# Optimization experiments

Measured on AMD Instinct MI355X. Metric: run time of the kernel, lower is better.

## Reference

```python
import jax, jax.numpy as jnp
import numpy as np

N, F, H, C, CLS = 100000, 128, 4, 32, 2
E = 1600000
NEG_SLOPE = 0.2


def setup_inputs() -> dict:
    key = jax.random.key(0)
    ks = jax.random.split(key, 8)
    x = jax.random.normal(ks[0], (N, F), dtype=jnp.float32)
    edge_index = jax.random.randint(ks[1], (2, E), 0, N, dtype=jnp.int64)
    # GATConv params (PyG layout): lin weight [H*C, F], att vectors [H, C], bias [H*C]
    W_gat = jax.random.normal(ks[2], (H * C, F), dtype=jnp.float32) * (1.0 / np.sqrt(F))
    att_src = jax.random.normal(ks[3], (H, C), dtype=jnp.float32) * (1.0 / np.sqrt(C))
    att_dst = jax.random.normal(ks[4], (H, C), dtype=jnp.float32) * (1.0 / np.sqrt(C))
    b_gat = jnp.zeros((H * C,), dtype=jnp.float32)
    # final classifier Linear(H*C -> CLS)
    W_lin = jax.random.normal(ks[5], (CLS, H * C), dtype=jnp.float32) * (1.0 / np.sqrt(H * C))
    b_lin = jnp.zeros((CLS,), dtype=jnp.float32)
    return {"x": x, "edge_index": edge_index, "W_gat": W_gat, "att_src": att_src,
            "att_dst": att_dst, "b_gat": b_gat, "W_lin": W_lin, "b_lin": b_lin}


def _gat_conv(x, edge_index, W_gat, att_src, att_dst, b_gat):
    # add self loops (PyG default add_self_loops=True)
    loop = jnp.arange(N, dtype=edge_index.dtype)
    src = jnp.concatenate([edge_index[0], loop])  # [E+N]
    dst = jnp.concatenate([edge_index[1], loop])
    h = (x @ W_gat.T).reshape(N, H, C)            # [N, H, C]
    a_src = jnp.einsum('nhc,hc->nh', h, att_src)  # [N, H]
    a_dst = jnp.einsum('nhc,hc->nh', h, att_dst)
    e = a_src[src] + a_dst[dst]                   # [E+N, H]
    e = jnp.where(e >= 0, e, NEG_SLOPE * e)       # leaky_relu(0.2)
    # segment softmax over incoming edges of each destination node
    m = jax.ops.segment_max(e, dst, num_segments=N)          # [N, H]
    ex = jnp.exp(e - m[dst])                                  # [E+N, H]
    denom = jax.ops.segment_sum(ex, dst, num_segments=N)      # [N, H]
    alpha = ex / denom[dst]                                    # [E+N, H]
    msg = alpha[:, :, None] * h[src]                           # [E+N, H, C]
    out = jax.ops.segment_sum(msg, dst, num_segments=N)       # [N, H, C]
    return out.reshape(N, H * C) + b_gat


def reference(x, edge_index, W_gat, att_src, att_dst, b_gat, W_lin, b_lin):
    out = _gat_conv(x, edge_index, W_gat, att_src, att_dst, b_gat)
    out = jax.nn.relu(out)
    return out @ W_lin.T + b_lin  # [N, CLS]
```

## Files before the change

kernel.cpp:

```cpp
#include <hip/hip_runtime.h>

#define NSLOPE  0.2f
#define LEXP(v) __expf((v) >= 0.f ? (v) : NSLOPE * (v))

typedef __attribute__((ext_vector_type(8))) short bf16x8;
typedef __attribute__((ext_vector_type(4))) float f32x4;

__device__ __forceinline__ unsigned bf16_rne(float f) {
    unsigned x = __float_as_uint(f);
    return (x + 0x7fffu + ((x >> 16) & 1u)) >> 16;
}
__device__ __forceinline__ float bf_lo(unsigned u) { return __uint_as_float(u << 16); }
__device__ __forceinline__ float bf_hi(unsigned u) { return __uint_as_float(u & 0xffff0000u); }

__global__ __launch_bounds__(256) void k_gemm_init(
    const float* __restrict__ x, const float* __restrict__ Wg,
    const float* __restrict__ att_src, const float* __restrict__ att_dst,
    unsigned* __restrict__ h2, float* __restrict__ a_src, float* __restrict__ a_dst,
    int N, int* __restrict__ gcur, int nbkt, int cap)
{
    __shared__ unsigned short Wl[128 * 136];
    __shared__ unsigned short wattH[8][128];

    const int t = threadIdx.x;

    if (blockIdx.x >= 512) {
        for (int i = t; i < nbkt; i += 256) gcur[i] = i * cap;
        return;
    }

    for (int i = t; i < 128 * 32; i += 256) {
        int r = i >> 5, c4 = (i & 31) * 4;
        float4 w = *(const float4*)(Wg + r * 128 + c4);
        unsigned* wp = (unsigned*)((char*)Wl + r * 272 + c4 * 2);
        wp[0] = bf16_rne(w.x) | (bf16_rne(w.y) << 16);
        wp[1] = bf16_rne(w.z) | (bf16_rne(w.w) << 16);
    }
    for (int idx = t; idx < 1024; idx += 256) {
        int j = idx >> 7, f = idx & 127;
        const float* av = (j < 4) ? (att_src + j * 32) : (att_dst + (j - 4) * 32);
        int hh = (j & 3) * 32;
        float s = 0.f;
        #pragma unroll 8
        for (int k = 0; k < 32; ++k)
            s += av[k] * Wg[(size_t)(hh + k) * 128 + f];
        wattH[j][f] = (unsigned short)bf16_rne(s);
    }
    __syncthreads();

    const int wave = t >> 6, l = t & 63;
    const int col = l & 15, kg = l >> 4;

    union { bf16x8 v; unsigned short s[8]; } batt[4];
    #pragma unroll
    for (int s4 = 0; s4 < 4; ++s4) {
        #pragma unroll
        for (int jj = 0; jj < 8; ++jj)
            batt[s4].s[jj] = (col < 8) ? wattH[col][s4 * 32 + kg * 8 + jj]
                                       : (unsigned short)0;
    }

    const int nwaves = 512 * 4;
    const int wid = blockIdx.x * 4 + wave;

    for (int mb = wid * 16; mb < N; mb += nwaves * 16) {
        union { bf16x8 v; unsigned u[4]; } af[4];
        int row = mb + col; if (row >= N) row = N - 1;
        const float* xr = x + (size_t)row * 128 + kg * 8;
        #pragma unroll
        for (int s = 0; s < 4; ++s) {
            float4 xa = *(const float4*)(xr + s * 32);
            float4 xb = *(const float4*)(xr + s * 32 + 4);
            af[s].u[0] = bf16_rne(xa.x) | (bf16_rne(xa.y) << 16);
            af[s].u[1] = bf16_rne(xa.z) | (bf16_rne(xa.w) << 16);
            af[s].u[2] = bf16_rne(xb.x) | (bf16_rne(xb.y) << 16);
            af[s].u[3] = bf16_rne(xb.z) | (bf16_rne(xb.w) << 16);
        }

        f32x4 acc[8];
        #pragma unroll
        for (int tl = 0; tl < 8; ++tl) acc[tl] = (f32x4){0.f, 0.f, 0.f, 0.f};
        f32x4 accd = (f32x4){0.f, 0.f, 0.f, 0.f};

        #pragma unroll
        for (int s = 0; s < 4; ++s) {
            #pragma unroll
            for (int tl = 0; tl < 8; ++tl) {
                const bf16x8 bf = *(const bf16x8*)((char*)Wl
                    + (tl * 16 + col) * 272 + (s * 32 + kg * 8) * 2);
                acc[tl] = __builtin_amdgcn_mfma_f32_16x16x32_bf16(af[s].v, bf, acc[tl], 0, 0, 0);
            }
            accd = __builtin_amdgcn_mfma_f32_16x16x32_bf16(af[s].v, batt[s].v, accd, 0, 0, 0);
        }

        #pragma unroll
        for (int tl = 0; tl < 4; ++tl) {
            #pragma unroll
            for (int r = 0; r < 4; ++r) {
                int node = mb + kg * 4 + r;
                if (node < N) {
                    unsigned w = bf16_rne(acc[tl][r]) | (bf16_rne(acc[tl + 4][r]) << 16);
                    h2[(size_t)node * 64 + tl * 16 + col] = w;
                }
            }
        }
        if (col < 8) {
            float* bp = (col < 4) ? a_src : a_dst;
            const int j = col & 3;
            #pragma unroll
            for (int r = 0; r < 4; ++r) {
                int node = mb + kg * 4 + r;
                if (node < N) bp[(size_t)node * 4 + j] = accd[r];
            }
        }
    }
}

__global__ __launch_bounds__(256) void k_partB2(
    const int* __restrict__ ei, int* __restrict__ gcur,
    unsigned* __restrict__ stage, int E, int nbkt, int chunk)
{
    __shared__ int dstc[6272];
    __shared__ int lcnt[1600];
    __shared__ int lbase[1600];
    const int t = threadIdx.x;
    for (int i = t; i < nbkt; i += 256) lcnt[i] = 0;
    __syncthreads();
    const int lo = blockIdx.x * chunk, hi = min(lo + chunk, E);
    for (int e = lo + t; e < hi; e += 256) {
        int d = ei[E + e];
        dstc[e - lo] = d;
        atomicAdd(&lcnt[d >> 6], 1);
    }
    __syncthreads();
    for (int i = t; i < nbkt; i += 256) {
        int c = lcnt[i];
        lbase[i] = (c > 0) ? atomicAdd(&gcur[i], c) : 0;
    }
    __syncthreads();
    for (int e = lo + t; e < hi; e += 256) {
        int s = ei[e];
        int d = dstc[e - lo];
        int pos = atomicAdd(&lbase[d >> 6], 1);
        stage[pos] = (unsigned)s | ((unsigned)(d & 63) << 26);
    }
}

__global__ __launch_bounds__(512) void k_aggC(
    const unsigned* __restrict__ stage, const int* __restrict__ gcur,
    const float* __restrict__ a_src, const float* __restrict__ a_dst,
    const unsigned* __restrict__ h2, const float* __restrict__ b_gat,
    const float* __restrict__ W_lin, const float* __restrict__ b_lin,
    float* __restrict__ out, int N, int cap)
{
    __shared__ int      eS[1728];
    __shared__ unsigned eA0[1728];
    __shared__ unsigned eA1[1728];
    __shared__ int cnt[64];
    __shared__ int cur[64];
    __shared__ int rs[64];
    __shared__ int re[64];
    __shared__ float adl[64][4];

    const int b = blockIdx.x, t = threadIdx.x;
    const int wave = t >> 6, l = t & 63;

    if (t < 64) {
        cnt[t] = 0;
        int n = (b << 6) + t;
        float4 v = (n < N) ? *(const float4*)(a_dst + (size_t)n * 4)
                           : make_float4(0.f, 0.f, 0.f, 0.f);
        *(float4*)adl[t] = v;
    }
    __syncthreads();
    const int slo = b * cap;
    const int ecnt = gcur[b] - slo;
    for (int e = t; e < ecnt; e += 512)
        atomicAdd(&cnt[stage[slo + e] >> 26], 1);
    __syncthreads();
    if (t < 64) {
        int v = cnt[t];
        int pv = (v + 7) & ~7;
        int sc = pv;
        #pragma unroll
        for (int m = 1; m < 64; m <<= 1) {
            int u = __shfl_up(sc, m);
            if (t >= m) sc += u;
        }
        int c0 = sc - pv;
        cur[t] = c0;
        rs[t] = c0; re[t] = c0 + pv;
    }
    __syncthreads();
    for (int e = t; e < ecnt; e += 512) {
        unsigned u = stage[slo + e];
        int s  = (int)(u & 0x3FFFFFFu);
        int dl = (int)(u >> 26);
        float4 av = *(const float4*)(a_src + (size_t)s * 4);
        float x0 = LEXP(av.x + adl[dl][0]);
        float x1 = LEXP(av.y + adl[dl][1]);
        float x2 = LEXP(av.z + adl[dl][2]);
        float x3 = LEXP(av.w + adl[dl][3]);
        int pos = atomicAdd(&cur[dl], 1);
        eS[pos]  = s;
        eA0[pos] = bf16_rne(x0) | (bf16_rne(x2) << 16);
        eA1[pos] = bf16_rne(x1) | (bf16_rne(x3) << 16);
    }
    __syncthreads();
    if (t < 64) {
        int n = (b << 6) + t;
        if (n < N) {
            const int e1 = cur[t], pe = re[t];
            for (int i = e1; i < pe; ++i) {
                eS[i] = n; eA0[i] = 0u; eA1[i] = 0u;
            }
        }
    }
    __syncthreads();

    const int m    = l & 31;
    const int half = l >> 5;
    const int cch  = 2 * m;
    const int hsel = m >> 4;
    const unsigned* eAh = hsel ? eA1 : eA0;

    for (int ln = wave; ln < 64; ln += 8) {
        int n = (b << 6) + ln;
        if (n >= N) break;
        const int start = rs[ln], end = re[ln];
        float a00 = 0.f, a01 = 0.f, a10 = 0.f, a11 = 0.f;
        float dA = 0.f, dB = 0.f;

        int i = start;
        for (; i + 16 <= end; i += 16) {
            int sk[8]; unsigned d[8]; uint2 u[8];
            #pragma unroll
            for (int k = 0; k < 8; ++k) {
                int j = i + 2 * k + half;
                sk[k] = eS[j];
                d[k]  = eAh[j];
            }
            #pragma unroll
            for (int k = 0; k < 8; ++k)
                u[k] = *(const uint2*)(h2 + (size_t)sk[k] * 64 + cch);
            #pragma unroll
            for (int k = 0; k < 8; ++k) {
                float wl = bf_lo(d[k]), wh = bf_hi(d[k]);
                dA += wl; dB += wh;
                a00 += wl * bf_lo(u[k].x); a01 += wh * bf_hi(u[k].x);
                a10 += wl * bf_lo(u[k].y); a11 += wh * bf_hi(u[k].y);
            }
        }
        if (i < end) {
            int sk[4]; unsigned d[4]; uint2 u[4];
            #pragma unroll
            for (int k = 0; k < 4; ++k) {
                int j = i + 2 * k + half;
                sk[k] = eS[j];
                d[k]  = eAh[j];
            }
            #pragma unroll
            for (int k = 0; k < 4; ++k)
                u[k] = *(const uint2*)(h2 + (size_t)sk[k] * 64 + cch);
            #pragma unroll
            for (int k = 0; k < 4; ++k) {
                float wl = bf_lo(d[k]), wh = bf_hi(d[k]);
                dA += wl; dB += wh;
                a00 += wl * bf_lo(u[k].x); a01 += wh * bf_hi(u[k].x);
                a10 += wl * bf_lo(u[k].y); a11 += wh * bf_hi(u[k].y);
            }
        }

        a00 += __shfl_xor(a00, 32);
        a01 += __shfl_xor(a01, 32);
        a10 += __shfl_xor(a10, 32);
        a11 += __shfl_xor(a11, 32);
        dA  += __shfl_xor(dA, 32);
        dB  += __shfl_xor(dB, 32);

        {
            float sA = LEXP(a_src[(size_t)n * 4 + hsel]     + adl[ln][hsel]);
            float sB = LEXP(a_src[(size_t)n * 4 + 2 + hsel] + adl[ln][2 + hsel]);
            uint2 u = *(const uint2*)(h2 + (size_t)n * 64 + cch);
            a00 += sA * bf_lo(u.x); a01 += sB * bf_hi(u.x);
            a10 += sA * bf_lo(u.y); a11 += sB * bf_hi(u.y);
            dA += sA; dB += sB;
        }
        const float ivA = 1.f / dA, ivB = 1.f / dB;
        a00 *= ivA; a01 *= ivB; a10 *= ivA; a11 *= ivB;

        float r0 = fmaxf(a00 + b_gat[cch],      0.f);
        float r1 = fmaxf(a01 + b_gat[cch + 64], 0.f);
        float r2 = fmaxf(a10 + b_gat[cch + 1],  0.f);
        float r3 = fmaxf(a11 + b_gat[cch + 65], 0.f);
        float p0 = r0 * W_lin[cch]       + r1 * W_lin[cch + 64]
                 + r2 * W_lin[cch + 1]   + r3 * W_lin[cch + 65];
        float p1 = r0 * W_lin[128 + cch]     + r1 * W_lin[128 + cch + 64]
                 + r2 * W_lin[128 + cch + 1] + r3 * W_lin[128 + cch + 65];
        #pragma unroll
        for (int s = 1; s < 32; s <<= 1) {
            p0 += __shfl_xor(p0, s);
            p1 += __shfl_xor(p1, s);
        }
        if (l == 0) {
            out[(size_t)n * 2]     = p0 + b_lin[0];
            out[(size_t)n * 2 + 1] = p1 + b_lin[1];
        }
    }
}

extern "C" void kernel_launch(void* const* d_in, const int* in_sizes, int n_in,
                              void* d_out, int out_size, void* d_ws, size_t ws_size,
                              hipStream_t stream)
{
    const float* x       = (const float*)d_in[0];
    const int*   ei      = (const int*)d_in[1];
    const float* Wg      = (const float*)d_in[2];
    const float* att_src = (const float*)d_in[3];
    const float* att_dst = (const float*)d_in[4];
    const float* b_gat   = (const float*)d_in[5];
    const float* W_lin   = (const float*)d_in[6];
    const float* b_lin   = (const float*)d_in[7];
    float* out = (float*)d_out;

    const int N = in_sizes[0] / 128;
    const int E = in_sizes[1] / 2;
    const int NBKT = (N + 63) >> 6;
    const int CAP  = 1728;
    const int NBLKB = 256;
    const int CHUNK = (E + NBLKB - 1) / NBLKB;

    char* ws = (char*)d_ws;
    unsigned* h2  = (unsigned*)ws;
    float* a_src  = (float*)(h2 + (size_t)N * 64);
    float* a_dst  = a_src + (size_t)N * 4;
    unsigned* stage = (unsigned*)(a_dst + (size_t)N * 4);
    int*   gcur   = (int*)(stage + (size_t)NBKT * CAP);

    k_gemm_init<<<513, 256, 0, stream>>>(
        x, Wg, att_src, att_dst, h2, a_src, a_dst, N, gcur, NBKT, CAP);
    k_partB2<<<NBLKB, 256, 0, stream>>>(ei, gcur, stage, E, NBKT, CHUNK);
    k_aggC<<<NBKT, 512, 0, stream>>>(stage, gcur, a_src, a_dst, h2,
                                     b_gat, W_lin, b_lin, out, N, CAP);
}
```

Before: 135.0 us.

## Split bf16 feature table into two head-pair halves and gather in two passes

```diff
diff --git a/kernel.cpp b/kernel.cpp
--- a/kernel.cpp
+++ b/kernel.cpp
@@ -16,7 +16,8 @@
 __global__ __launch_bounds__(256) void k_gemm_init(
     const float* __restrict__ x, const float* __restrict__ Wg,
     const float* __restrict__ att_src, const float* __restrict__ att_dst,
-    unsigned* __restrict__ h2, float* __restrict__ a_src, float* __restrict__ a_dst,
+    unsigned* __restrict__ h2a, unsigned* __restrict__ h2b,
+    float* __restrict__ a_src, float* __restrict__ a_dst,
     int N, int* __restrict__ gcur, int nbkt, int cap)
 {
     __shared__ unsigned short Wl[128 * 136];
@@ -94,13 +95,15 @@
         }
 
         #pragma unroll
-        for (int tl = 0; tl < 4; ++tl) {
+        for (int tl = 0; tl < 2; ++tl) {
             #pragma unroll
             for (int r = 0; r < 4; ++r) {
                 int node = mb + kg * 4 + r;
                 if (node < N) {
-                    unsigned w = bf16_rne(acc[tl][r]) | (bf16_rne(acc[tl + 4][r]) << 16);
-                    h2[(size_t)node * 64 + tl * 16 + col] = w;
+                    h2a[(size_t)node * 32 + tl * 16 + col] =
+                        bf16_rne(acc[tl][r]) | (bf16_rne(acc[tl + 2][r]) << 16);
+                    h2b[(size_t)node * 32 + tl * 16 + col] =
+                        bf16_rne(acc[tl + 4][r]) | (bf16_rne(acc[tl + 6][r]) << 16);
                 }
             }
         }
@@ -149,9 +152,9 @@
 __global__ __launch_bounds__(512) void k_aggC(
     const unsigned* __restrict__ stage, const int* __restrict__ gcur,
     const float* __restrict__ a_src, const float* __restrict__ a_dst,
-    const unsigned* __restrict__ h2, const float* __restrict__ b_gat,
-    const float* __restrict__ W_lin, const float* __restrict__ b_lin,
-    float* __restrict__ out, int N, int cap)
+    const unsigned* __restrict__ h2a, const unsigned* __restrict__ h2b,
+    const float* __restrict__ b_gat, const float* __restrict__ W_lin,
+    const float* __restrict__ b_lin, float* __restrict__ out, int N, int cap)
 {
     __shared__ int      eS[1728];
     __shared__ unsigned eA0[1728];
@@ -161,6 +164,7 @@
     __shared__ int rs[64];
     __shared__ int re[64];
     __shared__ float adl[64][4];
+    __shared__ float c01L[64][2][32];
 
     const int b = blockIdx.x, t = threadIdx.x;
     const int wave = t >> 6, l = t & 63;
@@ -218,85 +222,127 @@
     }
     __syncthreads();
 
-    const int m    = l & 31;
+    const int mch  = l & 31;
     const int half = l >> 5;
-    const int cch  = 2 * m;
-    const int hsel = m >> 4;
-    const unsigned* eAh = hsel ? eA1 : eA0;
 
     for (int ln = wave; ln < 64; ln += 8) {
         int n = (b << 6) + ln;
         if (n >= N) break;
         const int start = rs[ln], end = re[ln];
-        float a00 = 0.f, a01 = 0.f, a10 = 0.f, a11 = 0.f;
-        float dA = 0.f, dB = 0.f;
+        float s0 = 0.f, s1 = 0.f, d0 = 0.f, d1 = 0.f;
 
         int i = start;
         for (; i + 16 <= end; i += 16) {
-            int sk[8]; unsigned d[8]; uint2 u[8];
+            int sk[8]; unsigned a0[8], a1[8], u[8];
             #pragma unroll
             for (int k = 0; k < 8; ++k) {
                 int j = i + 2 * k + half;
-                sk[k] = eS[j];
-                d[k]  = eAh[j];
+                sk[k] = eS[j]; a0[k] = eA0[j]; a1[k] = eA1[j];
             }
             #pragma unroll
             for (int k = 0; k < 8; ++k)
-                u[k] = *(const uint2*)(h2 + (size_t)sk[k] * 64 + cch);
+                u[k] = h2a[(size_t)sk[k] * 32 + mch];
             #pragma unroll
             for (int k = 0; k < 8; ++k) {
-                float wl = bf_lo(d[k]), wh = bf_hi(d[k]);
-                dA += wl; dB += wh;
-                a00 += wl * bf_lo(u[k].x); a01 += wh * bf_hi(u[k].x);
-                a10 += wl * bf_lo(u[k].y); a11 += wh * bf_hi(u[k].y);
+                float w0 = bf_lo(a0[k]), w1 = bf_lo(a1[k]);
+                d0 += w0; d1 += w1;
+                s0 += w0 * bf_lo(u[k]); s1 += w1 * bf_hi(u[k]);
             }
         }
         if (i < end) {
-            int sk[4]; unsigned d[4]; uint2 u[4];
+            int sk[4]; unsigned a0[4], a1[4], u[4];
             #pragma unroll
             for (int k = 0; k < 4; ++k) {
                 int j = i + 2 * k + half;
-                sk[k] = eS[j];
-                d[k]  = eAh[j];
+                sk[k] = eS[j]; a0[k] = eA0[j]; a1[k] = eA1[j];
             }
             #pragma unroll
             for (int k = 0; k < 4; ++k)
-                u[k] = *(const uint2*)(h2 + (size_t)sk[k] * 64 + cch);
+                u[k] = h2a[(size_t)sk[k] * 32 + mch];
             #pragma unroll
             for (int k = 0; k < 4; ++k) {
-                float wl = bf_lo(d[k]), wh = bf_hi(d[k]);
-                dA += wl; dB += wh;
-                a00 += wl * bf_lo(u[k].x); a01 += wh * bf_hi(u[k].x);
-                a10 += wl * bf_lo(u[k].y); a11 += wh * bf_hi(u[k].y);
-            }
-        }
-
-        a00 += __shfl_xor(a00, 32);
-        a01 += __shfl_xor(a01, 32);
-        a10 += __shfl_xor(a10, 32);
-        a11 += __shfl_xor(a11, 32);
-        dA  += __shfl_xor(dA, 32);
-        dB  += __shfl_xor(dB, 32);
-
+                float w0 = bf_lo(a0[k]), w1 = bf_lo(a1[k]);
+                d0 += w0; d1 += w1;
+                s0 += w0 * bf_lo(u[k]); s1 += w1 * bf_hi(u[k]);
+            }
+        }
+
+        s0 += __shfl_xor(s0, 32); s1 += __shfl_xor(s1, 32);
+        d0 += __shfl_xor(d0, 32); d1 += __shfl_xor(d1, 32);
         {
-            float sA = LEXP(a_src[(size_t)n * 4 + hsel]     + adl[ln][hsel]);
-            float sB = LEXP(a_src[(size_t)n * 4 + 2 + hsel] + adl[ln][2 + hsel]);
-            uint2 u = *(const uint2*)(h2 + (size_t)n * 64 + cch);
-            a00 += sA * bf_lo(u.x); a01 += sB * bf_hi(u.x);
-            a10 += sA * bf_lo(u.y); a11 += sB * bf_hi(u.y);
-            dA += sA; dB += sB;
-        }
-        const float ivA = 1.f / dA, ivB = 1.f / dB;
-        a00 *= ivA; a01 *= ivB; a10 *= ivA; a11 *= ivB;
-
-        float r0 = fmaxf(a00 + b_gat[cch],      0.f);
-        float r1 = fmaxf(a01 + b_gat[cch + 64], 0.f);
-        float r2 = fmaxf(a10 + b_gat[cch + 1],  0.f);
-        float r3 = fmaxf(a11 + b_gat[cch + 65], 0.f);
-        float p0 = r0 * W_lin[cch]       + r1 * W_lin[cch + 64]
-                 + r2 * W_lin[cch + 1]   + r3 * W_lin[cch + 65];
-        float p1 = r0 * W_lin[128 + cch]     + r1 * W_lin[128 + cch + 64]
-                 + r2 * W_lin[128 + cch + 1] + r3 * W_lin[128 + cch + 65];
+            float sA = LEXP(a_src[(size_t)n * 4 + 0] + adl[ln][0]);
+            float sB = LEXP(a_src[(size_t)n * 4 + 1] + adl[ln][1]);
+            unsigned u = h2a[(size_t)n * 32 + mch];
+            s0 += sA * bf_lo(u); s1 += sB * bf_hi(u);
+            d0 += sA; d1 += sB;
+        }
+        if (half == 0) {
+            c01L[ln][0][mch] = s0 / d0;
+            c01L[ln][1][mch] = s1 / d1;
+        }
+    }
+
+    for (int ln = wave; ln < 64; ln += 8) {
+        int n = (b << 6) + ln;
+        if (n >= N) break;
+        const int start = rs[ln], end = re[ln];
+        float s2 = 0.f, s3 = 0.f, d2 = 0.f, d3 = 0.f;
+
+        int i = start;
+        for (; i + 16 <= end; i += 16) {
+            int sk[8]; unsigned a0[8], a1[8], u[8];
+            #pragma unroll
+            for (int k = 0; k < 8; ++k) {
+                int j = i + 2 * k + half;
+                sk[k] = eS[j]; a0[k] = eA0[j]; a1[k] = eA1[j];
+            }
+            #pragma unroll
+            for (int k = 0; k < 8; ++k)
+                u[k] = h2b[(size_t)sk[k] * 32 + mch];
+            #pragma unroll
+            for (int k = 0; k < 8; ++k) {
+                float w2 = bf_hi(a0[k]), w3 = bf_hi(a1[k]);
+                d2 += w2; d3 += w3;
+                s2 += w2 * bf_lo(u[k]); s3 += w3 * bf_hi(u[k]);
+            }
+        }
+        if (i < end) {
+            int sk[4]; unsigned a0[4], a1[4], u[4];
+            #pragma unroll
+            for (int k = 0; k < 4; ++k) {
+                int j = i + 2 * k + half;
+                sk[k] = eS[j]; a0[k] = eA0[j]; a1[k] = eA1[j];
+            }
+            #pragma unroll
+            for (int k = 0; k < 4; ++k)
+                u[k] = h2b[(size_t)sk[k] * 32 + mch];
+            #pragma unroll
+            for (int k = 0; k < 4; ++k) {
+                float w2 = bf_hi(a0[k]), w3 = bf_hi(a1[k]);
+                d2 += w2; d3 += w3;
+                s2 += w2 * bf_lo(u[k]); s3 += w3 * bf_hi(u[k]);
+            }
+        }
+
+        s2 += __shfl_xor(s2, 32); s3 += __shfl_xor(s3, 32);
+        d2 += __shfl_xor(d2, 32); d3 += __shfl_xor(d3, 32);
+        {
+            float sA = LEXP(a_src[(size_t)n * 4 + 2] + adl[ln][2]);
+            float sB = LEXP(a_src[(size_t)n * 4 + 3] + adl[ln][3]);
+            unsigned u = h2b[(size_t)n * 32 + mch];
+            s2 += sA * bf_lo(u); s3 += sB * bf_hi(u);
+            d2 += sA; d3 += sB;
+        }
+        s2 /= d2; s3 /= d3;
+
+        float r0 = fmaxf(c01L[ln][0][mch] + b_gat[mch],      0.f);
+        float r1 = fmaxf(c01L[ln][1][mch] + b_gat[mch + 32], 0.f);
+        float r2 = fmaxf(s2               + b_gat[mch + 64], 0.f);
+        float r3 = fmaxf(s3               + b_gat[mch + 96], 0.f);
+        float p0 = r0 * W_lin[mch]      + r1 * W_lin[mch + 32]
+                 + r2 * W_lin[mch + 64] + r3 * W_lin[mch + 96];
+        float p1 = r0 * W_lin[128 + mch]      + r1 * W_lin[128 + mch + 32]
+                 + r2 * W_lin[128 + mch + 64] + r3 * W_lin[128 + mch + 96];
         #pragma unroll
         for (int s = 1; s < 32; s <<= 1) {
             p0 += __shfl_xor(p0, s);
@@ -331,15 +377,16 @@
     const int CHUNK = (E + NBLKB - 1) / NBLKB;
 
     char* ws = (char*)d_ws;
-    unsigned* h2  = (unsigned*)ws;
-    float* a_src  = (float*)(h2 + (size_t)N * 64);
+    unsigned* h2a = (unsigned*)ws;
+    unsigned* h2b = h2a + (size_t)N * 32;
+    float* a_src  = (float*)(h2b + (size_t)N * 32);
     float* a_dst  = a_src + (size_t)N * 4;
     unsigned* stage = (unsigned*)(a_dst + (size_t)N * 4);
     int*   gcur   = (int*)(stage + (size_t)NBKT * CAP);
 
     k_gemm_init<<<513, 256, 0, stream>>>(
-        x, Wg, att_src, att_dst, h2, a_src, a_dst, N, gcur, NBKT, CAP);
+        x, Wg, att_src, att_dst, h2a, h2b, a_src, a_dst, N, gcur, NBKT, CAP);
     k_partB2<<<NBLKB, 256, 0, stream>>>(ei, gcur, stage, E, NBKT, CHUNK);
-    k_aggC<<<NBKT, 512, 0, stream>>>(stage, gcur, a_src, a_dst, h2,
+    k_aggC<<<NBKT, 512, 0, stream>>>(stage, gcur, a_src, a_dst, h2a, h2b,
                                      b_gat, W_lin, b_lin, out, N, CAP);
 }
```

Result: slower. 141.9 us (+5.1%).
